# Performance work log

Hardware: AMD Instinct MI355X
Metric: run time of the kernel (lower is better)

Reference implementation:

```python
import jax, jax.numpy as jnp
import numpy as np

DIM = 256

def setup_inputs() -> dict:
    key = jax.random.key(0)
    ks = jax.random.split(key, 7)
    B, S, D = 8, 4096, DIM
    scale = 1.0 / np.sqrt(D)
    x = jax.random.normal(ks[0], (B, S, D), dtype=jnp.float32)
    # torch Linear: y = x @ W.T + b, W is [out, in]
    Wq = jax.random.normal(ks[1], (D, D), dtype=jnp.float32) * scale
    Wk = jax.random.normal(ks[2], (D, D), dtype=jnp.float32) * scale
    Wv = jax.random.normal(ks[3], (D, D), dtype=jnp.float32) * scale
    bq = jax.random.normal(ks[4], (D,), dtype=jnp.float32) * 0.01
    bk = jax.random.normal(ks[5], (D,), dtype=jnp.float32) * 0.01
    bv = jax.random.normal(ks[6], (D,), dtype=jnp.float32) * 0.01
    return {"x": x, "Wq": Wq, "bq": bq, "Wk": Wk, "bk": bk, "Wv": Wv, "bv": bv}

def reference(x, Wq, bq, Wk, bk, Wv, bv):
    D = x.shape[-1]
    scale = D ** -0.5
    q = jnp.einsum('bsd,ed->bse', x, Wq) + bq  # [B,S,D]
    k = jnp.einsum('bsd,ed->bse', x, Wk) + bk
    v = jnp.einsum('bsd,ed->bse', x, Wv) + bv
    attn = jnp.einsum('bqd,bkd->bqk', q, k) * scale  # [B,S,S]
    attn = jax.nn.softmax(attn, axis=-1)
    return x + jnp.einsum('bqk,bkd->bqd', attn, v)
```

## Files before the change

kernel.cpp:

```cpp
#include <hip/hip_runtime.h>
#include <hip/hip_bf16.h>

typedef __attribute__((ext_vector_type(8))) short bf16x8;
typedef __attribute__((ext_vector_type(4))) short short4v;
typedef __attribute__((ext_vector_type(4))) float f32x4;
typedef __attribute__((ext_vector_type(16))) float f32x16;

#define MFMA16(a, b, c) __builtin_amdgcn_mfma_f32_16x16x32_bf16(a, b, c, 0, 0, 0)
#define MFMA32(a, b, c) __builtin_amdgcn_mfma_f32_32x32x16_bf16(a, b, c, 0, 0, 0)

__device__ __forceinline__ short f2bf(float f) {
    union { __hip_bfloat16 h; short s; } u;
    u.h = __float2bfloat16(f);
    return u.s;
}

__device__ __forceinline__ bf16x8 cvt8(const float* __restrict__ p) {
    f32x4 a = *reinterpret_cast<const f32x4*>(p);
    f32x4 b = *reinterpret_cast<const f32x4*>(p + 4);
    bf16x8 r;
    r[0] = f2bf(a[0]); r[1] = f2bf(a[1]); r[2] = f2bf(a[2]); r[3] = f2bf(a[3]);
    r[4] = f2bf(b[0]); r[5] = f2bf(b[1]); r[6] = f2bf(b[2]); r[7] = f2bf(b[3]);
    return r;
}

typedef __attribute__((address_space(1))) const unsigned int g_u32;
typedef __attribute__((address_space(3))) unsigned int l_u32;
__device__ __forceinline__ void gld16(const void* g, void* l) {
    __builtin_amdgcn_global_load_lds((g_u32*)(g), (l_u32*)(l), 16, 0, 0);
}

#define SBAR()    asm volatile("s_barrier" ::: "memory")
#define VMCNT(N)  asm volatile("s_waitcnt vmcnt(" #N ")" ::: "memory")

__global__ void wcvt_kernel(const float* __restrict__ Wq, const float* __restrict__ Wk,
                            const float* __restrict__ Wv, short* __restrict__ Wb)
{
    int t = blockIdx.x * 256 + threadIdx.x;
    int out_row = t & 255;
    int h  = (t >> 8) & 1;
    int kc = (t >> 9) & 15;
    int proj = t >> 13;
    const float* src = (proj == 0 ? Wq : (proj == 1 ? Wk : Wv))
                     + out_row * 256 + kc * 16 + h * 8;
    *reinterpret_cast<bf16x8*>(Wb + t * 8) = cvt8(src);
}

__global__ __launch_bounds__(256, 2) void qkv_kernel(
    const float* __restrict__ x, const short* __restrict__ Wb,
    const float* __restrict__ bq, const float* __restrict__ bk, const float* __restrict__ bv,
    short* __restrict__ qo, short* __restrict__ ko, short* __restrict__ vto)
{
    const int wave = threadIdx.x >> 6, lane = threadIdx.x & 63;
    const int l31 = lane & 31, h = lane >> 5;
    const int row0 = blockIdx.x * 128;
    const int wrow = row0 + wave * 32;

    bf16x8 af[16];
    const float* __restrict__ xr = x + (size_t)(wrow + l31) * 256 + h * 8;
#pragma unroll
    for (int kc = 0; kc < 16; ++kc) af[kc] = cvt8(xr + kc * 16);

    __shared__ short tile[128][264];

    for (int proj = 0; proj < 3; ++proj) {
        const short* __restrict__ W = Wb + proj * 65536;
        const float* __restrict__ bias = proj == 0 ? bq : (proj == 1 ? bk : bv);

        f32x16 acc[8];
#pragma unroll
        for (int df = 0; df < 8; ++df)
#pragma unroll
            for (int e = 0; e < 16; ++e) acc[df][e] = 0.f;

#pragma unroll
        for (int kc = 0; kc < 16; ++kc)
#pragma unroll
            for (int df = 0; df < 8; ++df) {
                bf16x8 bfr = *reinterpret_cast<const bf16x8*>(
                    W + ((kc * 2 + h) * 256 + df * 32 + l31) * 8);
                acc[df] = MFMA32(af[kc], bfr, acc[df]);
            }

        if (proj < 2) {
            short* __restrict__ dst = proj == 0 ? qo : ko;
#pragma unroll
            for (int df = 0; df < 8; ++df) {
                int col = df * 32 + l31;
                float bv_ = bias[col];
#pragma unroll
                for (int rg = 0; rg < 16; ++rg) {
                    int r = (rg & 3) + 8 * (rg >> 2) + 4 * h;
                    dst[(size_t)(wrow + r) * 256 + col] = f2bf(acc[df][rg] + bv_);
                }
            }
        } else {
#pragma unroll
            for (int df = 0; df < 8; ++df) {
                int col = df * 32 + l31;
                float bv_ = bias[col];
#pragma unroll
                for (int rg = 0; rg < 16; ++rg) {
                    int r = (rg & 3) + 8 * (rg >> 2) + 4 * h;
                    tile[wave * 32 + r][col] = f2bf(acc[df][rg] + bv_);
                }
            }
            __syncthreads();
            int d = threadIdx.x;
            int bb = row0 >> 12, s0 = row0 & 4095;
            short* __restrict__ dst = vto + ((size_t)bb * 256 + d) * 4096 + s0;
#pragma unroll
            for (int i = 0; i < 16; ++i) {
                bf16x8 v;
#pragma unroll
                for (int j = 0; j < 8; ++j) {
                    int p  = i * 8 + j;
                    int kp = p & 63;
                    int key = (kp & 3) * 16 + (kp >> 2);
                    v[j] = tile[(p & 64) + key][d];
                }
                *reinterpret_cast<bf16x8*>(dst + i * 8) = v;
            }
        }
    }
}

__global__ __launch_bounds__(512, 2) void attn_kernel(
    const short* __restrict__ q, const short* __restrict__ k,
    const short* __restrict__ vt, const float* __restrict__ x,
    float* __restrict__ out)
{
    const int id = blockIdx.x;
    const int b = id & 7, qt = id >> 3;
    const int tid = threadIdx.x;
    const int wave = tid >> 6, lane = tid & 63;
    const int l15 = lane & 15, l4 = lane >> 4;
    const int qrow0 = qt * 128 + wave * 16;

    const short* __restrict__ qb = q  + (size_t)b * 4096 * 256;
    const short* __restrict__ kb = k  + (size_t)b * 4096 * 256;
    const short* __restrict__ vb = vt + (size_t)b * 256 * 4096;

    __shared__ short smemA[32768];
    __shared__ short smemB[32768];
    __shared__ short plds[8][16][72];
    short (*pw)[72] = plds[wave];

    bf16x8 qf[8];
    const short* __restrict__ qr = qb + (size_t)(qrow0 + l15) * 256 + l4 * 8;
#pragma unroll
    for (int kc = 0; kc < 8; ++kc)
        qf[kc] = *reinterpret_cast<const bf16x8*>(qr + kc * 32);

    f32x4 o[16];
#pragma unroll
    for (int df = 0; df < 16; ++df) { f32x4 z = {0.f,0.f,0.f,0.f}; o[df] = z; }

    float ls[4] = {0.f, 0.f, 0.f, 0.f};
    const float cs = 0.0625f * 1.44269504f;

#define STAGE(T, BUF)                                                          \
  { _Pragma("unroll")                                                          \
    for (int i = 0; i < 8; ++i) {                                              \
        int c = i * 512 + tid;                                                 \
        int ss = c & 63;                                                       \
        const short* src;                                                      \
        if (c < 2048) {                                                        \
            int nf = c >> 9, kc = (c >> 6) & 7;                                \
            src = kb + (size_t)((T) * 64 + nf * 16 + (ss & 15)) * 256          \
                     + kc * 32 + (ss >> 4) * 8;                                \
        } else {                                                               \
            int df = (c >> 7) & 15, kc2 = (c >> 6) & 1;                        \
            src = vb + (size_t)(df * 16 + (ss & 15)) * 4096 + (T) * 64         \
                     + kc2 * 32 + (ss >> 4) * 8;                               \
        }                                                                      \
        gld16(src, &BUF[c * 8]);                                               \
    } }

#define COMPUTE(BUF)                                                           \
  {                                                                            \
    f32x4 sacc[4];                                                             \
    _Pragma("unroll")                                                          \
    for (int nf = 0; nf < 4; ++nf) { f32x4 z = {0.f,0.f,0.f,0.f}; sacc[nf] = z; } \
    _Pragma("unroll")                                                          \
    for (int nf = 0; nf < 4; ++nf)                                             \
        _Pragma("unroll")                                                      \
        for (int kc = 0; kc < 8; ++kc) {                                       \
            bf16x8 kf = *reinterpret_cast<const bf16x8*>(                      \
                BUF + (nf * 512 + kc * 64 + lane) * 8);                        \
            sacc[nf] = MFMA16(qf[kc], kf, sacc[nf]);                           \
        }                                                                      \
    _Pragma("unroll")                                                          \
    for (int r = 0; r < 4; ++r) {                                              \
        short4v pk;                                                            \
        _Pragma("unroll")                                                      \
        for (int nf = 0; nf < 4; ++nf) {                                       \
            float p = exp2f(sacc[nf][r] * cs);                                 \
            ls[r] += p;                                                        \
            pk[nf] = f2bf(p);                                                  \
        }                                                                      \
        *reinterpret_cast<short4v*>(&pw[l4 * 4 + r][l15 * 4]) = pk;            \
    }                                                                          \
    bf16x8 pf0 = *reinterpret_cast<const bf16x8*>(&pw[l15][l4 * 8]);           \
    bf16x8 pf1 = *reinterpret_cast<const bf16x8*>(&pw[l15][32 + l4 * 8]);      \
    _Pragma("unroll")                                                          \
    for (int df = 0; df < 16; ++df) {                                          \
        bf16x8 v0 = *reinterpret_cast<const bf16x8*>(                          \
            BUF + 16384 + (df * 128 + lane) * 8);                              \
        bf16x8 v1 = *reinterpret_cast<const bf16x8*>(                          \
            BUF + 16384 + (df * 128 + 64 + lane) * 8);                         \
        o[df] = MFMA16(pf0, v0, o[df]);                                        \
        o[df] = MFMA16(pf1, v1, o[df]);                                        \
    }                                                                          \
  }

    STAGE(0, smemA);
    VMCNT(0);
    SBAR();
    __builtin_amdgcn_sched_barrier(0);

    for (int tt = 0; tt < 32; ++tt) {
        const int t1 = 2 * tt + 1;

        STAGE(2 * tt + 1, smemB);
        COMPUTE(smemA);
        VMCNT(0);
        SBAR();
        __builtin_amdgcn_sched_barrier(0);

        if (t1 < 63) STAGE(t1 + 1, smemA);
        COMPUTE(smemB);
        if (t1 < 63) VMCNT(0);
        SBAR();
        __builtin_amdgcn_sched_barrier(0);
    }

    float inv[4];
#pragma unroll
    for (int r = 0; r < 4; ++r) {
        float v = ls[r];
#pragma unroll
        for (int d = 1; d < 16; d <<= 1) v += __shfl_xor(v, d);
        inv[r] = 1.0f / v;
    }
#pragma unroll
    for (int r = 0; r < 4; ++r) {
        size_t row = (size_t)b * 4096 + qrow0 + l4 * 4 + r;
#pragma unroll
        for (int df = 0; df < 16; ++df) {
            int col = df * 16 + l15;
            out[row * 256 + col] = o[df][r] * inv[r] + x[row * 256 + col];
        }
    }
#undef STAGE
#undef COMPUTE
}

extern "C" void kernel_launch(void* const* d_in, const int* in_sizes, int n_in,
                              void* d_out, int out_size, void* d_ws, size_t ws_size,
                              hipStream_t stream) {
    const float* x  = (const float*)d_in[0];
    const float* Wq = (const float*)d_in[1];
    const float* bq = (const float*)d_in[2];
    const float* Wk = (const float*)d_in[3];
    const float* bk = (const float*)d_in[4];
    const float* Wv = (const float*)d_in[5];
    const float* bv = (const float*)d_in[6];
    float* out = (float*)d_out;

    char* ws = (char*)d_ws;
    short* qb  = (short*)ws;
    short* kb  = (short*)(ws + (size_t)16 * 1024 * 1024);
    short* vtb = (short*)(ws + (size_t)32 * 1024 * 1024);
    short* Wb  = (short*)d_out;

    wcvt_kernel<<<96, 256, 0, stream>>>(Wq, Wk, Wv, Wb);

    qkv_kernel<<<256, 256, 0, stream>>>(x, Wb, bq, bk, bv, qb, kb, vtb);

    attn_kernel<<<256, 512, 0, stream>>>(qb, kb, vtb, x, out);
}
```

Measured before the change: 291.3 us.

## Split attention key tiles across wave halves and merge partial outputs

Each block now handles 64 query rows instead of 128. The two halves of its waves each process half of every 64-key tile, and the partial P·V accumulators and row sums are combined through shared memory at the end. The grid doubles to 512 blocks, which gives more parallelism across CUs. The V-transpose key permutation in the QKV kernel is removed to match the new P layout. The cost is that each block loads K/V tiles for half as many queries, doubling total K/V staging traffic, plus an extra reduction step.

Result: slower. 394.7 us (+35.5%).

```diff
diff --git a/kernel.cpp b/kernel.cpp
--- a/kernel.cpp
+++ b/kernel.cpp
@@ -2,7 +2,6 @@
 #include <hip/hip_bf16.h>
 
 typedef __attribute__((ext_vector_type(8))) short bf16x8;
-typedef __attribute__((ext_vector_type(4))) short short4v;
 typedef __attribute__((ext_vector_type(4))) float f32x4;
 typedef __attribute__((ext_vector_type(16))) float f32x16;
 
@@ -113,12 +112,7 @@
             for (int i = 0; i < 16; ++i) {
                 bf16x8 v;
 #pragma unroll
-                for (int j = 0; j < 8; ++j) {
-                    int p  = i * 8 + j;
-                    int kp = p & 63;
-                    int key = (kp & 3) * 16 + (kp >> 2);
-                    v[j] = tile[(p & 64) + key][d];
-                }
+                for (int j = 0; j < 8; ++j) v[j] = tile[i * 8 + j][d];
                 *reinterpret_cast<bf16x8*>(dst + i * 8) = v;
             }
         }
@@ -135,7 +129,8 @@
     const int tid = threadIdx.x;
     const int wave = tid >> 6, lane = tid & 63;
     const int l15 = lane & 15, l4 = lane >> 4;
-    const int qrow0 = qt * 128 + wave * 16;
+    const int qg = wave & 3, hh = wave >> 2;
+    const int qrow0 = qt * 64 + qg * 16;
 
     const short* __restrict__ qb = q  + (size_t)b * 4096 * 256;
     const short* __restrict__ kb = k  + (size_t)b * 4096 * 256;
@@ -143,8 +138,8 @@
 
     __shared__ short smemA[32768];
     __shared__ short smemB[32768];
-    __shared__ short plds[8][16][72];
-    short (*pw)[72] = plds[wave];
+    __shared__ short plds[8][16][40];
+    short (*pw)[40] = plds[wave];
 
     bf16x8 qf[8];
     const short* __restrict__ qr = qb + (size_t)(qrow0 + l15) * 256 + l4 * 8;
@@ -179,38 +174,31 @@
 
 #define COMPUTE(BUF)                                                           \
   {                                                                            \
-    f32x4 sacc[4];                                                             \
-    _Pragma("unroll")                                                          \
-    for (int nf = 0; nf < 4; ++nf) { f32x4 z = {0.f,0.f,0.f,0.f}; sacc[nf] = z; } \
-    _Pragma("unroll")                                                          \
-    for (int nf = 0; nf < 4; ++nf)                                             \
+    f32x4 sacc[2];                                                             \
+    _Pragma("unroll")                                                          \
+    for (int nf = 0; nf < 2; ++nf) { f32x4 z = {0.f,0.f,0.f,0.f}; sacc[nf] = z; } \
+    _Pragma("unroll")                                                          \
+    for (int nf = 0; nf < 2; ++nf)                                             \
         _Pragma("unroll")                                                      \
         for (int kc = 0; kc < 8; ++kc) {                                       \
             bf16x8 kf = *reinterpret_cast<const bf16x8*>(                      \
-                BUF + (nf * 512 + kc * 64 + lane) * 8);                        \
+                BUF + ((hh * 2 + nf) * 512 + kc * 64 + lane) * 8);             \
             sacc[nf] = MFMA16(qf[kc], kf, sacc[nf]);                           \
         }                                                                      \
     _Pragma("unroll")                                                          \
-    for (int r = 0; r < 4; ++r) {                                              \
-        short4v pk;                                                            \
+    for (int nf = 0; nf < 2; ++nf)                                             \
         _Pragma("unroll")                                                      \
-        for (int nf = 0; nf < 4; ++nf) {                                       \
+        for (int r = 0; r < 4; ++r) {                                          \
             float p = exp2f(sacc[nf][r] * cs);                                 \
             ls[r] += p;                                                        \
-            pk[nf] = f2bf(p);                                                  \
+            pw[l4 * 4 + r][nf * 16 + l15] = f2bf(p);                           \
         }                                                                      \
-        *reinterpret_cast<short4v*>(&pw[l4 * 4 + r][l15 * 4]) = pk;            \
-    }                                                                          \
-    bf16x8 pf0 = *reinterpret_cast<const bf16x8*>(&pw[l15][l4 * 8]);           \
-    bf16x8 pf1 = *reinterpret_cast<const bf16x8*>(&pw[l15][32 + l4 * 8]);      \
+    bf16x8 pf = *reinterpret_cast<const bf16x8*>(&pw[l15][l4 * 8]);            \
     _Pragma("unroll")                                                          \
     for (int df = 0; df < 16; ++df) {                                          \
-        bf16x8 v0 = *reinterpret_cast<const bf16x8*>(                          \
-            BUF + 16384 + (df * 128 + lane) * 8);                              \
-        bf16x8 v1 = *reinterpret_cast<const bf16x8*>(                          \
-            BUF + 16384 + (df * 128 + 64 + lane) * 8);                         \
-        o[df] = MFMA16(pf0, v0, o[df]);                                        \
-        o[df] = MFMA16(pf1, v1, o[df]);                                        \
+        bf16x8 vf = *reinterpret_cast<const bf16x8*>(                          \
+            BUF + 16384 + (df * 128 + hh * 64 + lane) * 8);                    \
+        o[df] = MFMA16(pf, vf, o[df]);                                         \
     }                                                                          \
   }
 
@@ -235,21 +223,43 @@
         __builtin_amdgcn_sched_barrier(0);
     }
 
-    float inv[4];
 #pragma unroll
     for (int r = 0; r < 4; ++r) {
         float v = ls[r];
 #pragma unroll
         for (int d = 1; d < 16; d <<= 1) v += __shfl_xor(v, d);
-        inv[r] = 1.0f / v;
-    }
-#pragma unroll
-    for (int r = 0; r < 4; ++r) {
-        size_t row = (size_t)b * 4096 + qrow0 + l4 * 4 + r;
+        ls[r] = v;
+    }
+
+    f32x4* __restrict__ fo = (f32x4*)smemA;
+    float* __restrict__ fl = (float*)plds;
+
+    __syncthreads();
+
+    if (hh == 1) {
+#pragma unroll
+        for (int df = 0; df < 16; ++df)
+            fo[(qg * 16 + df) * 64 + lane] = o[df];
+#pragma unroll
+        for (int r = 0; r < 4; ++r)
+            fl[(qg * 4 + r) * 64 + lane] = ls[r];
+    }
+    __syncthreads();
+
+    if (hh == 0) {
+        float inv[4];
+#pragma unroll
+        for (int r = 0; r < 4; ++r)
+            inv[r] = 1.0f / (ls[r] + fl[(qg * 4 + r) * 64 + lane]);
 #pragma unroll
         for (int df = 0; df < 16; ++df) {
+            f32x4 od = fo[(qg * 16 + df) * 64 + lane];
             int col = df * 16 + l15;
-            out[row * 256 + col] = o[df][r] * inv[r] + x[row * 256 + col];
+#pragma unroll
+            for (int r = 0; r < 4; ++r) {
+                size_t row = (size_t)b * 4096 + qrow0 + l4 * 4 + r;
+                out[row * 256 + col] = (o[df][r] + od[r]) * inv[r] + x[row * 256 + col];
+            }
         }
     }
 #undef STAGE
@@ -278,5 +288,5 @@
 
     qkv_kernel<<<256, 256, 0, stream>>>(x, Wb, bq, bk, bv, qb, kb, vtb);
 
-    attn_kernel<<<256, 512, 0, stream>>>(qb, kb, vtb, x, out);
-}
+    attn_kernel<<<512, 512, 0, stream>>>(qb, kb, vtb, x, out);
+}
```
